# Kernel tuning notes

Measured on AMD Instinct MI355X. Metric: run time of the kernel, lower is better.

The kernel has to match this reference:

```python
import jax, jax.numpy as jnp
import numpy as np

B, S, E = 1, 2048, 4096
H, D = 32, 128  # num_heads, head_dim


def setup_inputs() -> dict:
    key = jax.random.key(0)
    k1, k2, k3 = jax.random.split(key, 3)
    hidden_states = jax.random.normal(k1, (B, S, E), dtype=jnp.float32)
    # real RoPE tables (half-rotation / llama-style), base 10000
    inv_freq = 1.0 / (10000.0 ** (np.arange(0, D, 2, dtype=np.float32) / D))  # [D/2]
    pos = np.arange(S, dtype=np.float32)
    freqs = np.outer(pos, inv_freq)                      # [S, D/2]
    emb = np.concatenate([freqs, freqs], axis=-1)        # [S, D]
    cos = jnp.asarray(np.cos(emb), dtype=jnp.float32)
    sin = jnp.asarray(np.sin(emb), dtype=jnp.float32)
    w_pack = jax.random.normal(k2, (3 * E, E), dtype=jnp.float32) * (E ** -0.5)
    w_o = jax.random.normal(k3, (E, E), dtype=jnp.float32) * (E ** -0.5)
    return {"hidden_states": hidden_states, "cos": cos, "sin": sin,
            "w_pack": w_pack, "w_o": w_o}


def _rotate_half(x):
    x1, x2 = jnp.split(x, 2, axis=-1)
    return jnp.concatenate([-x2, x1], axis=-1)


def reference(hidden_states, cos, sin, w_pack, w_o):
    # fused QKV projection (W_pack, no bias)
    qkv = jnp.einsum('bse,fe->bsf', hidden_states, w_pack)      # [B,S,3E]
    q, k, v = jnp.split(qkv, 3, axis=-1)
    q = q.reshape(B, S, H, D)
    k = k.reshape(B, S, H, D)
    v = v.reshape(B, S, H, D)
    # RoPE (7B path; is_13b=False)
    c = cos[None, :, None, :]
    s = sin[None, :, None, :]
    q = q * c + _rotate_half(q) * s
    k = k * c + _rotate_half(k) * s
    # causal attention (prefill, empty past KV cache)
    scale = 1.0 / jnp.sqrt(jnp.asarray(D, dtype=q.dtype))
    scores = jnp.einsum('bqhd,bkhd->bhqk', q, k) * scale        # [B,H,S,S]
    causal = jnp.tril(jnp.ones((S, S), dtype=bool))
    scores = jnp.where(causal[None, None], scores, jnp.asarray(-1e30, scores.dtype))
    probs = jax.nn.softmax(scores, axis=-1)
    attn = jnp.einsum('bhqk,bkhd->bqhd', probs, v)              # [B,S,H,D]
    attn = attn.reshape(B, S, H * D)
    # output projection
    return jnp.einsum('bsf,ef->bse', attn, w_o)
```

## Files before the change

kernel.cpp:

```cpp
#include <hip/hip_runtime.h>

typedef unsigned short u16;
typedef unsigned int   u32;
typedef __attribute__((ext_vector_type(8))) short short8;
typedef __attribute__((ext_vector_type(4))) float f32x4;

__device__ __forceinline__ float b2f(u16 u) {
  union { float f; u32 i; } v; v.i = ((u32)u) << 16; return v.f;
}
__device__ __forceinline__ u16 f2b(float f) {
  union { float f; u32 i; } v; v.f = f;
  u32 r = v.i + 0x7fffu + ((v.i >> 16) & 1u);
  return (u16)(r >> 16);
}

__device__ __forceinline__ void gload_lds16(const void* g, void* l) {
  __builtin_amdgcn_global_load_lds(
      (const __attribute__((address_space(1))) void*)g,
      (__attribute__((address_space(3))) void*)l, 16, 0, 0);
}

template <int N> __device__ __forceinline__ void wait_vmcnt() {
  if constexpr (N == 0)      asm volatile("s_waitcnt vmcnt(0)" ::: "memory");
  else if constexpr (N == 2) asm volatile("s_waitcnt vmcnt(2)" ::: "memory");
  else if constexpr (N == 3) asm volatile("s_waitcnt vmcnt(3)" ::: "memory");
  else if constexpr (N == 6) asm volatile("s_waitcnt vmcnt(6)" ::: "memory");
  else static_assert(N < 0, "unsupported vmcnt literal");
}

__device__ __forceinline__ ushort4 cvt4(float4 v) {
  ushort4 o;
  o.x = f2b(v.x); o.y = f2b(v.y); o.z = f2b(v.z); o.w = f2b(v.w);
  return o;
}

__global__ __launch_bounds__(256) void cvt_hp(const float* __restrict__ hs,
                                              const float* __restrict__ wp,
                                              u16* __restrict__ h_bf,
                                              u16* __restrict__ wp_bf) {
  const long H4 = 2097152, W4 = 12582912;
  for (long i = (long)blockIdx.x * 256 + threadIdx.x; i < H4 + W4;
       i += (long)gridDim.x * 256) {
    if (i < H4)
      ((ushort4*)h_bf)[i] = cvt4(((const float4*)hs)[i]);
    else
      ((ushort4*)wp_bf)[i - H4] = cvt4(((const float4*)wp)[i - H4]);
  }
}

__global__ __launch_bounds__(256) void cvt_bf16(const float* __restrict__ in,
                                                u16* __restrict__ out, int n4) {
  for (long i = (long)blockIdx.x * 256 + threadIdx.x; i < n4; i += (long)gridDim.x * 256)
    ((ushort4*)out)[i] = cvt4(((const float4*)in)[i]);
}

__device__ __forceinline__ short8 frag_ld64(const u16* base, int rbase, int kk,
                                            int fr, int fq) {
  const int r = rbase + fr;
  return *(const short8*)(base + r * 64 + ((((kk << 2) + fq) ^ (r & 7)) << 3));
}

__global__ __launch_bounds__(512, 2) void gemm8p(const u16* __restrict__ A,
                                                 const u16* __restrict__ B,
                                                 u16* __restrict__ Cq,
                                                 u16* __restrict__ VT,
                                                 int M, int N, int K) {
  constexpr int AE = 16384;
  constexpr int BUFSZ = AE + 12288;
  __shared__ u16 lds[2 * BUFSZ];
  const int tid = threadIdx.x;
  const int wid = tid >> 6, lane = tid & 63;
  const int fr = lane & 15, fq = lane >> 4;
  const int mA = (wid >> 2) * 128;
  const int nB = (wid & 3) * 48;

  const int nty = M >> 8;
  const int qx = gridDim.x >> 3;
  const int wg = (blockIdx.x & 7) * qx + (blockIdx.x >> 3);
  const int by = wg % nty, bx = wg / nty;
  const long row0 = (long)by * 256, col0 = (long)bx * 192;

  const int rr8 = tid >> 3;
  const int jl = (tid & 7) ^ (rr8 & 7);
  const u16* gA = A + (row0 + rr8) * (long)K + jl * 8;
  const u16* gB = B + (col0 + rr8) * (long)K + jl * 8;

  f32x4 acc[8][3];
#pragma unroll
  for (int m = 0; m < 8; ++m)
#pragma unroll
    for (int n = 0; n < 3; ++n) acc[m][n] = f32x4{0.f, 0.f, 0.f, 0.f};

  const int NT = K >> 6;

  auto stageA = [&](int i, int t) {
    gload_lds16(gA + (long)(i * 64) * K + (long)t * 64,
                lds + (t & 1) * BUFSZ + (i * 512 + tid) * 8);
  };
  auto stageB = [&](int i, int t) {
    gload_lds16(gB + (long)(i * 64) * K + (long)t * 64,
                lds + (t & 1) * BUFSZ + AE + (i * 512 + tid) * 8);
  };

#pragma unroll
  for (int i = 0; i < 4; ++i) stageA(i, 0);
#pragma unroll
  for (int i = 0; i < 3; ++i) stageB(i, 0);
#pragma unroll
  for (int i = 0; i < 3; ++i) stageB(i, 1);
  wait_vmcnt<3>();
  __builtin_amdgcn_s_barrier();

  for (int t = 0; t < NT; ++t) {
    const u16* SA = lds + (t & 1) * BUFSZ;
    const u16* SB = SA + AE;
    short8 a0[4], a1[4], b0[3], b1[3];

#pragma unroll
    for (int m = 0; m < 4; ++m) a0[m] = frag_ld64(SA, mA + m * 16, 0, fr, fq);
#pragma unroll
    for (int n = 0; n < 3; ++n) b0[n] = frag_ld64(SB, nB + n * 16, 0, fr, fq);
#pragma unroll
    for (int n = 0; n < 3; ++n) b1[n] = frag_ld64(SB, nB + n * 16, 1, fr, fq);
    if (t + 1 < NT) { stageA(0, t + 1); stageA(1, t + 1); }
    __builtin_amdgcn_s_setprio(1);
#pragma unroll
    for (int m = 0; m < 4; ++m)
#pragma unroll
      for (int n = 0; n < 3; ++n)
        acc[m][n] = __builtin_amdgcn_mfma_f32_16x16x32_bf16(a0[m], b0[n], acc[m][n], 0, 0, 0);
    __builtin_amdgcn_s_setprio(0);
    asm volatile("s_waitcnt lgkmcnt(0)" ::: "memory");
    __builtin_amdgcn_s_barrier();

#pragma unroll
    for (int m = 0; m < 4; ++m) a1[m] = frag_ld64(SA, mA + 64 + m * 16, 0, fr, fq);
    if (t + 1 < NT) { stageA(2, t + 1); stageA(3, t + 1); }
    __builtin_amdgcn_s_setprio(1);
#pragma unroll
    for (int m = 0; m < 4; ++m)
#pragma unroll
      for (int n = 0; n < 3; ++n)
        acc[4 + m][n] = __builtin_amdgcn_mfma_f32_16x16x32_bf16(a1[m], b0[n], acc[4 + m][n], 0, 0, 0);
    __builtin_amdgcn_s_setprio(0);
    __builtin_amdgcn_s_barrier();

#pragma unroll
    for (int m = 0; m < 4; ++m) a0[m] = frag_ld64(SA, mA + m * 16, 1, fr, fq);
    if (t + 2 < NT) { stageB(0, t + 2); stageB(1, t + 2); }
    __builtin_amdgcn_s_setprio(1);
#pragma unroll
    for (int m = 0; m < 4; ++m)
#pragma unroll
      for (int n = 0; n < 3; ++n)
        acc[m][n] = __builtin_amdgcn_mfma_f32_16x16x32_bf16(a0[m], b1[n], acc[m][n], 0, 0, 0);
    __builtin_amdgcn_s_setprio(0);
    __builtin_amdgcn_s_barrier();

#pragma unroll
    for (int m = 0; m < 4; ++m) a1[m] = frag_ld64(SA, mA + 64 + m * 16, 1, fr, fq);
    if (t + 2 < NT) stageB(2, t + 2);
    __builtin_amdgcn_s_setprio(1);
#pragma unroll
    for (int m = 0; m < 4; ++m)
#pragma unroll
      for (int n = 0; n < 3; ++n)
        acc[4 + m][n] = __builtin_amdgcn_mfma_f32_16x16x32_bf16(a1[m], b1[n], acc[4 + m][n], 0, 0, 0);
    __builtin_amdgcn_s_setprio(0);
    if (t + 2 < NT) wait_vmcnt<3>();
    else            wait_vmcnt<0>();
    __builtin_amdgcn_s_barrier();
  }

#pragma unroll
  for (int m = 0; m < 8; ++m)
#pragma unroll
    for (int n = 0; n < 3; ++n) {
      const long c = col0 + nB + n * 16 + fr;
      const long rb = row0 + mA + m * 16 + fq * 4;
      if (c >= 8192) {
        ushort4 o;
        o.x = f2b(acc[m][n][0]); o.y = f2b(acc[m][n][1]);
        o.z = f2b(acc[m][n][2]); o.w = f2b(acc[m][n][3]);
        *(ushort4*)(VT + (c - 8192) * 2048 + rb) = o;
      } else {
#pragma unroll
        for (int j = 0; j < 4; ++j) Cq[(rb + j) * N + c] = f2b(acc[m][n][j]);
      }
    }
}

__global__ __launch_bounds__(512, 2) void gemm2_4p(const u16* __restrict__ A,
                                                   const u16* __restrict__ B,
                                                   float* __restrict__ C,
                                                   int M, int N, int K) {
  constexpr int AE = 16384;
  constexpr int BUFSZ = AE + 8192;
  __shared__ u16 lds[2 * BUFSZ];
  const int tid = threadIdx.x;
  const int wid = tid >> 6, lane = tid & 63;
  const int fr = lane & 15, fq = lane >> 4;
  const int mA = (wid >> 2) * 128;
  const int nB = (wid & 3) * 32;

  const int nty = M >> 8;
  const int qx = gridDim.x >> 3;
  const int wg = (blockIdx.x & 7) * qx + (blockIdx.x >> 3);
  const int by = wg % nty, bx = wg / nty;
  const long row0 = (long)by * 256, col0 = (long)bx * 128;

  const int rr8 = tid >> 3;
  const int jl = (tid & 7) ^ (rr8 & 7);
  const u16* gA = A + (row0 + rr8) * (long)K + jl * 8;
  const u16* gB = B + (col0 + rr8) * (long)K + jl * 8;

  f32x4 acc[8][2];
#pragma unroll
  for (int m = 0; m < 8; ++m)
#pragma unroll
    for (int n = 0; n < 2; ++n) acc[m][n] = f32x4{0.f, 0.f, 0.f, 0.f};

  const int NT = K >> 6;

  auto stageA = [&](int i, int t) {
    gload_lds16(gA + (long)(i * 64) * K + (long)t * 64,
                lds + (t & 1) * BUFSZ + (i * 512 + tid) * 8);
  };
  auto stageB = [&](int i, int t) {
    gload_lds16(gB + (long)(i * 64) * K + (long)t * 64,
                lds + (t & 1) * BUFSZ + AE + (i * 512 + tid) * 8);
  };

#pragma unroll
  for (int i = 0; i < 4; ++i) stageA(i, 0);
#pragma unroll
  for (int i = 0; i < 2; ++i) stageB(i, 0);
#pragma unroll
  for (int i = 0; i < 2; ++i) stageB(i, 1);
  wait_vmcnt<2>();
  __builtin_amdgcn_s_barrier();

  for (int t = 0; t < NT; ++t) {
    const u16* SA = lds + (t & 1) * BUFSZ;
    const u16* SB = SA + AE;
    short8 a0[4], a1[4], b0[2], b1[2];

#pragma unroll
    for (int m = 0; m < 4; ++m) a0[m] = frag_ld64(SA, mA + m * 16, 0, fr, fq);
#pragma unroll
    for (int n = 0; n < 2; ++n) b0[n] = frag_ld64(SB, nB + n * 16, 0, fr, fq);
#pragma unroll
    for (int n = 0; n < 2; ++n) b1[n] = frag_ld64(SB, nB + n * 16, 1, fr, fq);
    if (t + 1 < NT) { stageA(0, t + 1); stageA(1, t + 1); }
    __builtin_amdgcn_s_setprio(1);
#pragma unroll
    for (int m = 0; m < 4; ++m)
#pragma unroll
      for (int n = 0; n < 2; ++n)
        acc[m][n] = __builtin_amdgcn_mfma_f32_16x16x32_bf16(a0[m], b0[n], acc[m][n], 0, 0, 0);
    __builtin_amdgcn_s_setprio(0);
    asm volatile("s_waitcnt lgkmcnt(0)" ::: "memory");
    __builtin_amdgcn_s_barrier();

#pragma unroll
    for (int m = 0; m < 4; ++m) a1[m] = frag_ld64(SA, mA + 64 + m * 16, 0, fr, fq);
    if (t + 1 < NT) { stageA(2, t + 1); stageA(3, t + 1); }
    __builtin_amdgcn_s_setprio(1);
#pragma unroll
    for (int m = 0; m < 4; ++m)
#pragma unroll
      for (int n = 0; n < 2; ++n)
        acc[4 + m][n] = __builtin_amdgcn_mfma_f32_16x16x32_bf16(a1[m], b0[n], acc[4 + m][n], 0, 0, 0);
    __builtin_amdgcn_s_setprio(0);
    __builtin_amdgcn_s_barrier();

#pragma unroll
    for (int m = 0; m < 4; ++m) a0[m] = frag_ld64(SA, mA + m * 16, 1, fr, fq);
    if (t + 2 < NT) stageB(0, t + 2);
    __builtin_amdgcn_s_setprio(1);
#pragma unroll
    for (int m = 0; m < 4; ++m)
#pragma unroll
      for (int n = 0; n < 2; ++n)
        acc[m][n] = __builtin_amdgcn_mfma_f32_16x16x32_bf16(a0[m], b1[n], acc[m][n], 0, 0, 0);
    __builtin_amdgcn_s_setprio(0);
    __builtin_amdgcn_s_barrier();

#pragma unroll
    for (int m = 0; m < 4; ++m) a1[m] = frag_ld64(SA, mA + 64 + m * 16, 1, fr, fq);
    if (t + 2 < NT) stageB(1, t + 2);
    __builtin_amdgcn_s_setprio(1);
#pragma unroll
    for (int m = 0; m < 4; ++m)
#pragma unroll
      for (int n = 0; n < 2; ++n)
        acc[4 + m][n] = __builtin_amdgcn_mfma_f32_16x16x32_bf16(a1[m], b1[n], acc[4 + m][n], 0, 0, 0);
    __builtin_amdgcn_s_setprio(0);
    if (t + 2 < NT) wait_vmcnt<2>();
    else            wait_vmcnt<0>();
    __builtin_amdgcn_s_barrier();
  }

#pragma unroll
  for (int m = 0; m < 8; ++m)
#pragma unroll
    for (int n = 0; n < 2; ++n)
#pragma unroll
      for (int j = 0; j < 4; ++j) {
        const long r = row0 + mA + m * 16 + fq * 4 + j;
        const long c = col0 + nB + n * 16 + fr;
        C[r * N + c] = acc[m][n][j];
      }
}

__global__ __launch_bounds__(256) void rope_qk(u16* __restrict__ qkv,
                                               const float* __restrict__ cosb,
                                               const float* __restrict__ sinb) {
  const int idx = blockIdx.x * 256 + threadIdx.x;
  const int dq  = idx & 15;
  const int h   = (idx >> 4) & 31;
  const int seg = (idx >> 9) & 1;
  const int s   = idx >> 10;
  const int d0  = dq * 4;
  u16* base = qkv + (long)s * 12288 + seg * 4096 + h * 128;
  const ushort4 x1 = *(const ushort4*)(base + d0);
  const ushort4 x2 = *(const ushort4*)(base + d0 + 64);
  const float4 c1 = *(const float4*)(cosb + s * 128 + d0);
  const float4 s1 = *(const float4*)(sinb + s * 128 + d0);
  const float4 c2 = *(const float4*)(cosb + s * 128 + d0 + 64);
  const float4 s2 = *(const float4*)(sinb + s * 128 + d0 + 64);
  const float scale = seg ? 1.0f : 0.08838834764831845f;
  float x1f[4] = {b2f(x1.x), b2f(x1.y), b2f(x1.z), b2f(x1.w)};
  float x2f[4] = {b2f(x2.x), b2f(x2.y), b2f(x2.z), b2f(x2.w)};
  const float c1a[4] = {c1.x, c1.y, c1.z, c1.w}, s1a[4] = {s1.x, s1.y, s1.z, s1.w};
  const float c2a[4] = {c2.x, c2.y, c2.z, c2.w}, s2a[4] = {s2.x, s2.y, s2.z, s2.w};
  ushort4 o1, o2;
  u16* o1p = (u16*)&o1; u16* o2p = (u16*)&o2;
#pragma unroll
  for (int j = 0; j < 4; ++j) {
    o1p[j] = f2b((x1f[j] * c1a[j] - x2f[j] * s1a[j]) * scale);
    o2p[j] = f2b((x2f[j] * c2a[j] + x1f[j] * s2a[j]) * scale);
  }
  *(ushort4*)(base + d0) = o1;
  *(ushort4*)(base + d0 + 64) = o2;
}

__global__ __launch_bounds__(256) void attn_fwd(const u16* __restrict__ Qb,
                                                const u16* __restrict__ Kb,
                                                const u16* __restrict__ Vt,
                                                u16* __restrict__ Ob) {
  const int h = blockIdx.y;
  const int tid = threadIdx.x;
  const int wid = tid >> 6, lane = tid & 63;
  const int fr = lane & 15, fq = lane >> 4;

  __shared__ u16 Ks[2][64 * 128];
  __shared__ u16 Vts[2][128 * 64];
  __shared__ u16 Ps[4][32 * 72];

  auto stage = [&](int t, int buf) {
    const int kv0 = t * 64;
#pragma unroll
    for (int i = 0; i < 4; ++i) {
      const int c = wid * 4 + i;
      {
        const int r = c * 4 + (lane >> 4);
        const int p = lane & 15;
        const int jsrc = p ^ (r & 7);
        gload_lds16(Kb + (long)(kv0 + r) * 12288 + h * 128 + jsrc * 8,
                    (char*)Ks[buf] + c * 1024);
      }
      {
        const int d = c * 8 + (lane >> 3);
        const int p = lane & 7;
        const int jsrc = p ^ (d & 7);
        gload_lds16(Vt + (long)(h * 128 + d) * 2048 + kv0 + jsrc * 8,
                    (char*)Vts[buf] + c * 1024);
      }
    }
  };

#pragma unroll
  for (int pass = 0; pass < 2; ++pass) {
    const int qt = pass == 0 ? (int)blockIdx.x : 15 - (int)blockIdx.x;
    const int q0 = qt * 128;
    const int nt = 2 * qt + 2;
    const int wq_hi = q0 + wid * 32 + 31;

    short8 qf[2][4];
#pragma unroll
    for (int m = 0; m < 2; ++m) {
      const long qrow = q0 + wid * 32 + m * 16 + fr;
#pragma unroll
      for (int kk = 0; kk < 4; ++kk)
        qf[m][kk] = *(const short8*)(Qb + qrow * 12288 + h * 128 + kk * 32 + fq * 8);
    }

    f32x4 Oacc[2][8];
#pragma unroll
    for (int m = 0; m < 2; ++m)
#pragma unroll
      for (int f = 0; f < 8; ++f) Oacc[m][f] = f32x4{0.f, 0.f, 0.f, 0.f};
    float mrun[2][4], lrun[2][4];
#pragma unroll
    for (int m = 0; m < 2; ++m)
#pragma unroll
      for (int j = 0; j < 4; ++j) { mrun[m][j] = -1e30f; lrun[m][j] = 0.f; }

    stage(0, 0);
    wait_vmcnt<0>();
    __builtin_amdgcn_s_barrier();

    for (int t = 0; t < nt; ++t) {
      const int cur = t & 1;
      const int kv0 = t * 64;
      if (t + 1 < nt) stage(t + 1, cur ^ 1);

      if (kv0 <= wq_hi) {
        f32x4 S[2][4];
#pragma unroll
        for (int m = 0; m < 2; ++m)
#pragma unroll
          for (int n = 0; n < 4; ++n) S[m][n] = f32x4{0.f, 0.f, 0.f, 0.f};
#pragma unroll
        for (int kk = 0; kk < 4; ++kk) {
          short8 kf[4];
#pragma unroll
          for (int n = 0; n < 4; ++n) {
            const int r = n * 16 + fr;
            const int p = (kk * 4 + fq) ^ (r & 7);
            kf[n] = *(const short8*)((const char*)Ks[cur] + r * 256 + p * 16);
          }
#pragma unroll
          for (int m = 0; m < 2; ++m)
#pragma unroll
            for (int n = 0; n < 4; ++n)
              S[m][n] = __builtin_amdgcn_mfma_f32_16x16x32_bf16(qf[m][kk], kf[n], S[m][n], 0, 0, 0);
        }

        float P[2][4][4];
#pragma unroll
        for (int m = 0; m < 2; ++m) {
          float tm[4] = {-1e30f, -1e30f, -1e30f, -1e30f};
#pragma unroll
          for (int n = 0; n < 4; ++n) {
            const int kv = kv0 + n * 16 + fr;
#pragma unroll
            for (int j = 0; j < 4; ++j) {
              const int qi = q0 + wid * 32 + m * 16 + fq * 4 + j;
              const float s = (kv <= qi) ? S[m][n][j] : -1e30f;
              P[m][n][j] = s;
              tm[j] = fmaxf(tm[j], s);
            }
          }
#pragma unroll
          for (int j = 0; j < 4; ++j)
#pragma unroll
            for (int msk = 1; msk < 16; msk <<= 1)
              tm[j] = fmaxf(tm[j], __shfl_xor(tm[j], msk));

          float al[4], rs[4];
#pragma unroll
          for (int j = 0; j < 4; ++j) {
            const float mn = fmaxf(mrun[m][j], tm[j]);
            al[j] = __expf(mrun[m][j] - mn);
            mrun[m][j] = mn;
            rs[j] = 0.f;
          }
#pragma unroll
          for (int n = 0; n < 4; ++n)
#pragma unroll
            for (int j = 0; j < 4; ++j) {
              const float p = __expf(P[m][n][j] - mrun[m][j]);
              P[m][n][j] = p;
              rs[j] += p;
            }
#pragma unroll
          for (int j = 0; j < 4; ++j) {
#pragma unroll
            for (int msk = 1; msk < 16; msk <<= 1) rs[j] += __shfl_xor(rs[j], msk);
            lrun[m][j] = lrun[m][j] * al[j] + rs[j];
          }
#pragma unroll
          for (int f = 0; f < 8; ++f) {
            f32x4 o = Oacc[m][f];
#pragma unroll
            for (int j = 0; j < 4; ++j) o[j] *= al[j];
            Oacc[m][f] = o;
          }
        }

#pragma unroll
        for (int m = 0; m < 2; ++m)
#pragma unroll
          for (int n = 0; n < 4; ++n)
#pragma unroll
            for (int j = 0; j < 4; ++j)
              Ps[wid][(m * 16 + fq * 4 + j) * 72 + n * 16 + fr] = f2b(P[m][n][j]);

#pragma unroll
        for (int kb = 0; kb < 2; ++kb) {
          short8 pa0 = *(const short8*)(Ps[wid] + (fr) * 72 + kb * 32 + fq * 8);
          short8 pa1 = *(const short8*)(Ps[wid] + (16 + fr) * 72 + kb * 32 + fq * 8);
#pragma unroll
          for (int f = 0; f < 8; ++f) {
            const int d = f * 16 + fr;
            const int p = (kb * 4 + fq) ^ (d & 7);
            short8 vf = *(const short8*)((const char*)Vts[cur] + d * 128 + p * 16);
            Oacc[0][f] = __builtin_amdgcn_mfma_f32_16x16x32_bf16(pa0, vf, Oacc[0][f], 0, 0, 0);
            Oacc[1][f] = __builtin_amdgcn_mfma_f32_16x16x32_bf16(pa1, vf, Oacc[1][f], 0, 0, 0);
          }
        }
      }
      wait_vmcnt<0>();
      __builtin_amdgcn_s_barrier();
    }

#pragma unroll
    for (int m = 0; m < 2; ++m)
#pragma unroll
      for (int j = 0; j < 4; ++j) {
        const float inv = 1.f / lrun[m][j];
        const long r = q0 + wid * 32 + m * 16 + fq * 4 + j;
#pragma unroll
        for (int f = 0; f < 8; ++f)
          Ob[r * 4096 + h * 128 + f * 16 + fr] = f2b(Oacc[m][f][j] * inv);
      }
  }
}

extern "C" void kernel_launch(void* const* d_in, const int* in_sizes, int n_in,
                              void* d_out, int out_size, void* d_ws, size_t ws_size,
                              hipStream_t stream) {
  const float* hs   = (const float*)d_in[0];
  const float* cosb = (const float*)d_in[1];
  const float* sinb = (const float*)d_in[2];
  const float* wp   = (const float*)d_in[3];
  const float* wo   = (const float*)d_in[4];
  float* out = (float*)d_out;
  char* ws = (char*)d_ws;

  u16* h_bf  = (u16*)(ws);
  u16* attn  = (u16*)(ws);
  u16* wp_bf = (u16*)(ws + 16777216);
  u16* wo_bf = (u16*)(ws + 16777216);
  u16* qkv   = (u16*)(ws + 121634816);
  u16* vt    = (u16*)(ws + 171966464);

  cvt_hp<<<4096, 256, 0, stream>>>(hs, wp, h_bf, wp_bf);
  gemm8p<<<512, 512, 0, stream>>>(h_bf, wp_bf, qkv, vt, 2048, 12288, 4096);
  cvt_bf16<<<2048, 256, 0, stream>>>(wo, wo_bf, 4194304);
  rope_qk<<<8192, 256, 0, stream>>>(qkv, cosb, sinb);
  attn_fwd<<<dim3(8, 32), 256, 0, stream>>>(qkv, qkv + 4096, vt, attn);
  gemm2_4p<<<256, 512, 0, stream>>>(attn, wo_bf, out, 2048, 4096, 4096);
}
```

Before: 456.4 us.

## Triple-buffer attention K/V staging and fold W_o conversion into one cvt kernel

The attention kernel moves from double to triple buffering of K and V^T tiles in LDS. It prefetches two tiles ahead and waits with a partial vmcnt so global loads overlap more compute. Separately, the fp32-to-bf16 conversion of W_o is merged into the existing input conversion kernel, which removes one launch. To do that, workspace offsets are moved so W_o no longer aliases the W_pack buffer. The cost is more LDS per block (about 112KB), which may cut occupancy, and a larger workspace footprint.

```diff
diff --git a/kernel.cpp b/kernel.cpp
--- a/kernel.cpp
+++ b/kernel.cpp
@@ -25,6 +25,7 @@
   else if constexpr (N == 2) asm volatile("s_waitcnt vmcnt(2)" ::: "memory");
   else if constexpr (N == 3) asm volatile("s_waitcnt vmcnt(3)" ::: "memory");
   else if constexpr (N == 6) asm volatile("s_waitcnt vmcnt(6)" ::: "memory");
+  else if constexpr (N == 8) asm volatile("s_waitcnt vmcnt(8)" ::: "memory");
   else static_assert(N < 0, "unsupported vmcnt literal");
 }
 
@@ -34,24 +35,22 @@
   return o;
 }
 
-__global__ __launch_bounds__(256) void cvt_hp(const float* __restrict__ hs,
-                                              const float* __restrict__ wp,
-                                              u16* __restrict__ h_bf,
-                                              u16* __restrict__ wp_bf) {
-  const long H4 = 2097152, W4 = 12582912;
-  for (long i = (long)blockIdx.x * 256 + threadIdx.x; i < H4 + W4;
+__global__ __launch_bounds__(256) void cvt_all(const float* __restrict__ hs,
+                                               const float* __restrict__ wp,
+                                               const float* __restrict__ wo,
+                                               u16* __restrict__ h_bf,
+                                               u16* __restrict__ wp_bf,
+                                               u16* __restrict__ wo_bf) {
+  const long H4 = 2097152, W4 = 12582912, O4 = 4194304;
+  for (long i = (long)blockIdx.x * 256 + threadIdx.x; i < H4 + W4 + O4;
        i += (long)gridDim.x * 256) {
     if (i < H4)
       ((ushort4*)h_bf)[i] = cvt4(((const float4*)hs)[i]);
+    else if (i < H4 + W4)
+      ((ushort4*)wp_bf)[i - H4] = cvt4(((const float4*)wp)[i - H4]);
     else
-      ((ushort4*)wp_bf)[i - H4] = cvt4(((const float4*)wp)[i - H4]);
+      ((ushort4*)wo_bf)[i - H4 - W4] = cvt4(((const float4*)wo)[i - H4 - W4]);
   }
-}
-
-__global__ __launch_bounds__(256) void cvt_bf16(const float* __restrict__ in,
-                                                u16* __restrict__ out, int n4) {
-  for (long i = (long)blockIdx.x * 256 + threadIdx.x; i < n4; i += (long)gridDim.x * 256)
-    ((ushort4*)out)[i] = cvt4(((const float4*)in)[i]);
 }
 
 __device__ __forceinline__ short8 frag_ld64(const u16* base, int rbase, int kk,
@@ -354,8 +353,8 @@
   const int wid = tid >> 6, lane = tid & 63;
   const int fr = lane & 15, fq = lane >> 4;
 
-  __shared__ u16 Ks[2][64 * 128];
-  __shared__ u16 Vts[2][128 * 64];
+  __shared__ u16 Ks[3][64 * 128];
+  __shared__ u16 Vts[3][128 * 64];
   __shared__ u16 Ps[4][32 * 72];
 
   auto stage = [&](int t, int buf) {
@@ -408,13 +407,14 @@
       for (int j = 0; j < 4; ++j) { mrun[m][j] = -1e30f; lrun[m][j] = 0.f; }
 
     stage(0, 0);
-    wait_vmcnt<0>();
+    if (nt > 1) { stage(1, 1); wait_vmcnt<8>(); }
+    else        wait_vmcnt<0>();
     __builtin_amdgcn_s_barrier();
 
     for (int t = 0; t < nt; ++t) {
-      const int cur = t & 1;
+      const int cur = t % 3;
       const int kv0 = t * 64;
-      if (t + 1 < nt) stage(t + 1, cur ^ 1);
+      if (t + 2 < nt) stage(t + 2, (t + 2) % 3);
 
       if (kv0 <= wq_hi) {
         f32x4 S[2][4];
@@ -512,7 +512,8 @@
           }
         }
       }
-      wait_vmcnt<0>();
+      if (t + 2 < nt) wait_vmcnt<8>();
+      else            wait_vmcnt<0>();
       __builtin_amdgcn_s_barrier();
     }
 
@@ -543,13 +544,12 @@
   u16* h_bf  = (u16*)(ws);
   u16* attn  = (u16*)(ws);
   u16* wp_bf = (u16*)(ws + 16777216);
-  u16* wo_bf = (u16*)(ws + 16777216);
-  u16* qkv   = (u16*)(ws + 121634816);
-  u16* vt    = (u16*)(ws + 171966464);
-
-  cvt_hp<<<4096, 256, 0, stream>>>(hs, wp, h_bf, wp_bf);
+  u16* wo_bf = (u16*)(ws + 117440512);
+  u16* qkv   = (u16*)(ws + 150994944);
+  u16* vt    = (u16*)(ws + 201326592);
+
+  cvt_all<<<4096, 256, 0, stream>>>(hs, wp, wo, h_bf, wp_bf, wo_bf);
   gemm8p<<<512, 512, 0, stream>>>(h_bf, wp_bf, qkv, vt, 2048, 12288, 4096);
-  cvt_bf16<<<2048, 256, 0, stream>>>(wo, wo_bf, 4194304);
   rope_qk<<<8192, 256, 0, stream>>>(qkv, cosb, sinb);
   attn_fwd<<<dim3(8, 32), 256, 0, stream>>>(qkv, qkv + 4096, vt, attn);
   gemm2_4p<<<256, 512, 0, stream>>>(attn, wo_bf, out, 2048, 4096, 4096);
```

Result: slower. 467.1 us (+2.4%).
